# Optimization experiments

Hardware: AMD Instinct MI355X
Metric: run time of the kernel (lower is better)

## Reference

```python
import jax, jax.numpy as jnp
import numpy as np

# (multiplicity, dim=2l+1) per irreducible field, for both input and output
RS = [(8, 1), (8, 3), (8, 5)]
SIZE = 3          # conv kernel spatial size
B_EL = 2          # radial basis elements per (i,j) kernel block
EPS = 1e-5


def _se3_bn_conv(x, weight, bases):
    """Training-mode SE3BatchNorm stats fused into dynamic kernel build + conv3d.
    x: (B, C_in, D, H, W); weight: flat (sum mi*mj*b_el,);
    bases[i][j]: (b_el, di, dj, SIZE, SIZE, SIZE).
    """
    B = x.shape[0]
    means = []    # per scalar (d==1) field: (m,)
    scales = []   # per field: (m,) inverse-std factors
    ix = 0
    for m, d in RS:
        field = x[:, ix:ix + m * d].reshape(B, m, d, -1)
        ix += m * d
        if d == 1:
            mean = jax.lax.stop_gradient(field.mean(axis=-1).mean(axis=0).reshape(-1))
            field = field - mean.reshape(1, m, 1, 1)
            means.append(mean)
        # reduce='mean': sum over d, mean over spatial, mean over batch (detached)
        norm = jax.lax.stop_gradient(jnp.sum(field * field, axis=2).mean(axis=-1).mean(axis=0))
        scales.append((norm + EPS) ** -0.5)

    # Build normalized dynamic kernel blocks and compensating bias
    widx = 0
    row_blocks = []
    bias_parts = []
    for i, (mi, di) in enumerate(RS):
        col_blocks = []
        bia = jnp.zeros((mi * di,), x.dtype)
        imean = 0
        for j, (mj, dj) in enumerate(RS):
            basis = bases[i][j]                     # (b, di, dj, s, s, s)
            b = basis.shape[0]
            w = weight[widx:widx + mi * mj * b].reshape(mi, mj, b)
            widx += mi * mj * b
            w = w * scales[j][None, :, None]        # per-input-field BN rescale
            # block: (mi*di, mj*dj, s, s, s)
            block = jnp.einsum('uvb,bdexyz->udvexyz', w, basis)
            col_blocks.append(block.reshape(mi * di, mj * dj, SIZE, SIZE, SIZE))
            if di == 1 and dj == 1:
                mean = means[imean]
                imean += 1
                identity = basis.reshape(b, -1).sum(-1)         # (b,)
                corr = (w.reshape(-1, b) @ identity[:, None]).reshape(mi, mj)
                bia = bia - (corr @ mean[:, None]).reshape(-1)
        row_blocks.append(jnp.concatenate(col_blocks, axis=1))
        bias_parts.append(bia)
    kernel = jnp.concatenate(row_blocks, axis=0)    # (C_out, C_in, s, s, s)
    bias = jnp.concatenate(bias_parts)              # (C_out,)

    out = jax.lax.conv_general_dilated(
        x, kernel, window_strides=(1, 1, 1), padding='VALID',
        dimension_numbers=('NCDHW', 'OIDHW', 'NCDHW'))
    return out + bias[None, :, None, None, None]


def setup_inputs() -> dict:
    key = jax.random.key(0)
    k_x, k_w = jax.random.split(key)
    C = sum(m * d for m, d in RS)  # 72
    x = jax.random.normal(k_x, (8, C, 32, 32, 32), jnp.float32)
    total_w = sum(mi * mj * B_EL for mi, _ in RS for mj, _ in RS)  # 1152
    weight = jax.random.normal(k_w, (total_w,), jnp.float32) * 0.1
    inp = {'x': x, 'weight': weight}
    for i, (mi, di) in enumerate(RS):
        for j, (mj, dj) in enumerate(RS):
            kb = jax.random.fold_in(key, 100 + 10 * i + j)
            inp['basis_{}_{}'.format(i, j)] = jax.random.normal(
                kb, (B_EL, di, dj, SIZE, SIZE, SIZE), jnp.float32) / (SIZE ** 1.5)
    return inp


def reference(x, weight, basis_0_0, basis_0_1, basis_0_2,
              basis_1_0, basis_1_1, basis_1_2,
              basis_2_0, basis_2_1, basis_2_2):
    bases = [[basis_0_0, basis_0_1, basis_0_2],
             [basis_1_0, basis_1_1, basis_1_2],
             [basis_2_0, basis_2_1, basis_2_2]]
    return _se3_bn_conv(x, weight, bases)
```

## Files before the change

kernel.cpp:

```cpp
#include <hip/hip_runtime.h>
#include <hip/hip_fp16.h>
#include <math.h>

#define NCH 72
#define SP  32768
#define NBATCH 8
#define NTOT (NBATCH*SP)

#define WS_SUMX   0
#define WS_SUMSQ  72
#define WS_SCALE  144
#define WS_BIAS   216
#define WS_K      288

#define WS_XH_BYTES 323712
#define XH_ROW   2720
#define XH_PLANE 87040
#define XH_BATCH 2785280

typedef __attribute__((ext_vector_type(8))) _Float16 half8;
typedef __attribute__((ext_vector_type(4))) float float4v;
typedef __attribute__((ext_vector_type(4))) int int4v;

__device__ __forceinline__ void chmap(int c, int& f, int& m, int& d, int& dim) {
  if (c < 8)       { f = 0; m = c;          d = 0;          dim = 1; }
  else if (c < 32) { f = 1; m = (c - 8)/3;  d = (c - 8)%3;  dim = 3; }
  else             { f = 2; m = (c - 32)/5; d = (c - 32)%5; dim = 5; }
}

__global__ __launch_bounds__(256) void prepack_kernel(const float* __restrict__ x,
                                                      float* __restrict__ ws) {
  __shared__ __align__(16) short tile[256 * 88];
  __shared__ float segS[72][3], segQ[72][3];
  const int t    = threadIdx.x;
  const int z    = blockIdx.x >> 1;
  const int half = blockIdx.x & 1;
  const int b    = blockIdx.y;
  ushort* xh = (ushort*)((char*)ws + WS_XH_BYTES);
  const float* xb = x + (size_t)b * NCH * SP + z * 1024 + half * 512;

  const int ci_s = t % 72, seg = t / 72;
  float accS = 0.f, accQ = 0.f;

  *(int4v*)&tile[t * 88 + 72] = (int4v){0, 0, 0, 0};

  for (int c = 0; c < 2; ++c) {
    if (c) __syncthreads();
    #pragma unroll
    for (int cig = 0; cig < 18; ++cig) {
      float v0 = xb[(size_t)(cig*4 + 0) * SP + c * 256 + t];
      float v1 = xb[(size_t)(cig*4 + 1) * SP + c * 256 + t];
      float v2 = xb[(size_t)(cig*4 + 2) * SP + c * 256 + t];
      float v3 = xb[(size_t)(cig*4 + 3) * SP + c * 256 + t];
      short s4[4] = { (short)__half_as_short(__float2half(v0)),
                      (short)__half_as_short(__float2half(v1)),
                      (short)__half_as_short(__float2half(v2)),
                      (short)__half_as_short(__float2half(v3)) };
      *(int2*)&tile[t * 88 + cig * 4] = *(const int2*)s4;
    }
    __syncthreads();
    {
      ushort* gb = xh + (size_t)b * XH_BATCH + (size_t)(z * 32 + (half * 2 + c) * 8) * XH_ROW;
      #pragma unroll
      for (int j = 0; j < 10; ++j) {
        const int s   = t + j * 256;
        const int pos = s / 10, part = s - pos * 10;
        const int4v v = *(const int4v*)&tile[pos * 88 + part * 8];
        const int row = pos >> 5, xx = pos & 31;
        *(int4v*)(gb + (size_t)row * XH_ROW + xx * 80 + part * 8) = v;
      }
    }
    if (seg < 3) {
      const int p0 = seg * 86;
      const int pn = (seg == 2) ? 84 : 86;
      for (int i = 0; i < pn; ++i) {
        const float v = __half2float(__short_as_half(tile[(p0 + i) * 88 + ci_s]));
        accS += v; accQ += v * v;
      }
    }
  }
  if (seg < 3) { segS[ci_s][seg] = accS; segQ[ci_s][seg] = accQ; }
  __syncthreads();
  if (t < 144) {
    const int which = t / 72, ci = t % 72;
    const float v = which ? (segQ[ci][0] + segQ[ci][1] + segQ[ci][2])
                          : (segS[ci][0] + segS[ci][1] + segS[ci][2]);
    atomicAdd(&ws[(which ? WS_SUMSQ : WS_SUMX) + ci], v);
  }
}

__global__ __launch_bounds__(256) void build_half_kernel(const float* __restrict__ weight,
    float* __restrict__ ws,
    const float* __restrict__ b00, const float* __restrict__ b01, const float* __restrict__ b02,
    const float* __restrict__ b10, const float* __restrict__ b11, const float* __restrict__ b12,
    const float* __restrict__ b20, const float* __restrict__ b21, const float* __restrict__ b22) {
  const int tid = blockIdx.x * 256 + threadIdx.x;
  const float invN = 1.0f / (float)NTOT;
  if (tid < 315 * 512) {
    const int blk = tid >> 9;
    const int e   = tid & 511;
    const int tap = blk / 35;
    const int r   = blk - tap * 35;
    const int kc  = r / 5, cj = r - (r / 5) * 5;
    const int l   = e >> 3, j = e & 7;
    const int co  = cj * 16 + (l & 15);
    const int kk  = kc * 32 + ((l >> 4) << 3) + j;
    short val = 0;
    if (co < NCH && kk < 216) {
      const int dx = kk / 72, ci = kk - dx * 72;
      int fi, u, dd, di; chmap(co, fi, u, dd, di);
      int fj, v, ee, dj; chmap(ci, fj, v, ee, dj);
      const float* bs[9] = {b00, b01, b02, b10, b11, b12, b20, b21, b22};
      const float* basis = bs[fi * 3 + fj];
      float norm;
      if (ci < 8) {
        float m = ws[WS_SUMX + ci] * invN;
        norm = ws[WS_SUMSQ + ci] * invN - m * m;
      } else if (ci < 32) {
        int m0 = 8 + ((ci - 8) / 3) * 3;
        norm = (ws[WS_SUMSQ+m0] + ws[WS_SUMSQ+m0+1] + ws[WS_SUMSQ+m0+2]) * invN;
      } else {
        int m0 = 32 + ((ci - 32) / 5) * 5;
        norm = (ws[WS_SUMSQ+m0] + ws[WS_SUMSQ+m0+1] + ws[WS_SUMSQ+m0+2]
              + ws[WS_SUMSQ+m0+3] + ws[WS_SUMSQ+m0+4]) * invN;
      }
      const float sc = 1.0f / sqrtf(norm + 1e-5f);
      const float* wp = weight + (fi * 3 + fj) * 128 + (u * 8 + v) * 2;
      const float w0 = wp[0] * sc, w1 = wp[1] * sc;
      const int t = tap * 3 + dx;
      const float f = w0 * basis[(dd * dj + ee) * 27 + t]
                    + w1 * basis[((di + dd) * dj + ee) * 27 + t];
      val = __half_as_short(__float2half(f));
    }
    ((short*)(ws + WS_K))[tid] = val;
  }
  if (blockIdx.x == 0) {
    __shared__ float s_mean[8], s_scale[8];
    const int c = threadIdx.x;
    if (c < 8) {
      float m = ws[WS_SUMX + c] * invN;
      float norm = ws[WS_SUMSQ + c] * invN - m * m;
      s_mean[c]  = m;
      s_scale[c] = 1.0f / sqrtf(norm + 1e-5f);
    }
    __syncthreads();
    if (c < NCH) {
      float bia = 0.f;
      if (c < 8) {
        float id0 = 0.f, id1 = 0.f;
        #pragma unroll
        for (int t = 0; t < 27; ++t) { id0 += b00[t]; id1 += b00[27 + t]; }
        #pragma unroll
        for (int v = 0; v < 8; ++v) {
          float s  = s_scale[v];
          float w0 = weight[(c*8 + v)*2 + 0] * s;
          float w1 = weight[(c*8 + v)*2 + 1] * s;
          bia -= (w0 * id0 + w1 * id1) * s_mean[v];
        }
      }
      ws[WS_BIAS + c] = bia;
    }
  }
}

__global__ __launch_bounds__(256, 2) void conv_direct(const float* __restrict__ ws,
                                                      float* __restrict__ out) {
  __shared__ __align__(16) char Bsm[35840];

  const int lane = threadIdx.x & 63;
  const int wv   = threadIdx.x >> 6;
  const int lx   = lane & 15;
  const int q    = lane >> 4;
  const int i  = blockIdx.x;
  const int b  = i & 7;
  const int q2 = i >> 3;
  const int yt = q2 & 7;
  const int zp = q2 >> 3;
  const int y  = yt * 4 + wv;
  const int yc = (y > 29) ? 29 : y;
  const int zb = zp * 2;

  const char* xhb = (const char*)ws + WS_XH_BYTES + (size_t)b * (XH_BATCH * 2);
  const char* Kb  = (const char*)(ws + WS_K);
  const float* __restrict__ bias = ws + WS_BIAS;

  const int lb16 = lane * 16;

  float4v acc[2][2][5];
  #pragma unroll
  for (int sz = 0; sz < 2; ++sz)
    #pragma unroll
    for (int s = 0; s < 2; ++s)
      #pragma unroll
      for (int cj = 0; cj < 5; ++cj)
        acc[sz][s][cj] = (float4v){0.f, 0.f, 0.f, 0.f};

#define STAGE(TAP) {                                                              \
    const char* src_ = Kb + (size_t)(TAP) * 35840;                                \
    _Pragma("unroll")                                                             \
    for (int k = 0; k < 9; ++k) {                                                 \
      const int idx = (int)threadIdx.x + (k << 8);                                \
      if (idx < 2240) {                                                           \
        __builtin_amdgcn_global_load_lds(                                         \
          (const __attribute__((address_space(1))) void*)(src_ + (size_t)idx*16), \
          (__attribute__((address_space(3))) void*)(Bsm + ((k<<8) + (wv<<6))*16), \
          16, 0, 0);                                                              \
      }                                                                           \
    }                                                                             \
  }

#define LOADA(KC, A) {                                                            \
    const int kk0_ = (KC) * 32 + (q << 3);                                        \
    const int dx_  = (kk0_ >= 144) ? 2 : ((kk0_ >= 72) ? 1 : 0);                  \
    const int ao_  = (lx * 80 + kk0_ + 8 * dx_) * 2;                              \
    A[0] = *(const half8*)(r0T + ao_);                                            \
    A[1] = *(const half8*)(r0T + ao_ + 2560);                                     \
    A[2] = *(const half8*)(r1T + ao_);                                            \
    A[3] = *(const half8*)(r1T + ao_ + 2560);                                     \
  }

#define MFQ(A, BF, CJ)                                                                         \
    acc[0][0][CJ] = __builtin_amdgcn_mfma_f32_16x16x32_f16(A[0], BF, acc[0][0][CJ], 0,0,0);    \
    acc[0][1][CJ] = __builtin_amdgcn_mfma_f32_16x16x32_f16(A[1], BF, acc[0][1][CJ], 0,0,0);    \
    acc[1][0][CJ] = __builtin_amdgcn_mfma_f32_16x16x32_f16(A[2], BF, acc[1][0][CJ], 0,0,0);    \
    acc[1][1][CJ] = __builtin_amdgcn_mfma_f32_16x16x32_f16(A[3], BF, acc[1][1][CJ], 0,0,0);

#define GROUP(KC, AC, PRE) {                                                      \
    half8 bf0 = *(const half8*)(Bsm + ((KC)*5 + 0)*1024 + lb16);                  \
    half8 bf1 = *(const half8*)(Bsm + ((KC)*5 + 1)*1024 + lb16);                  \
    half8 bf2 = *(const half8*)(Bsm + ((KC)*5 + 2)*1024 + lb16);                  \
    half8 bf3 = *(const half8*)(Bsm + ((KC)*5 + 3)*1024 + lb16);                  \
    half8 bf4 = *(const half8*)(Bsm + ((KC)*5 + 4)*1024 + lb16);                  \
    PRE;                                                                          \
    __builtin_amdgcn_s_setprio(1);                                                \
    MFQ(AC, bf0, 0) MFQ(AC, bf1, 1) MFQ(AC, bf2, 2) MFQ(AC, bf3, 3) MFQ(AC, bf4, 4) \
    __builtin_amdgcn_s_setprio(0);                                                \
  }

  half8 A0[4], A1[4], A2[4];

  #pragma unroll 1
  for (int tap = 0; tap < 9; ++tap) {
    const int dz_ = tap / 3, dy_ = tap - dz_ * 3;
    const char* r0T = xhb + (size_t)(((zb + dz_) * 32) + (yc + dy_)) * (XH_ROW * 2);
    const char* r1T = r0T + (XH_PLANE * 2);

    if (tap) __builtin_amdgcn_s_barrier();
    STAGE(tap);
    __builtin_amdgcn_sched_barrier(0);
    LOADA(0, A0); LOADA(1, A1);
    __builtin_amdgcn_sched_barrier(0);
    asm volatile("s_waitcnt vmcnt(8)" ::: "memory");
    __builtin_amdgcn_s_barrier();
    __builtin_amdgcn_sched_barrier(0);

    GROUP(0, A0, LOADA(2, A2));
    GROUP(1, A1, LOADA(3, A0));
    GROUP(2, A2, LOADA(4, A1));
    GROUP(3, A0, LOADA(5, A2));
    GROUP(4, A1, LOADA(6, A0));
    GROUP(5, A2, (void)0);
    GROUP(6, A0, (void)0);
  }

#undef STAGE
#undef LOADA
#undef MFQ
#undef GROUP

  if (y < 30) {
    #pragma unroll
    for (int cj = 0; cj < 5; ++cj) {
      const int co = cj * 16 + lx;
      if (co < NCH) {
        const float bv = bias[co];
        #pragma unroll
        for (int sz = 0; sz < 2; ++sz) {
          float* ob = out + ((size_t)(b * NCH + co) * 30 + (zb + sz)) * 900 + y * 30;
          #pragma unroll
          for (int s = 0; s < 2; ++s) {
            const int x0 = s * 16 + q * 4;
            const float4v v = acc[sz][s][cj];
            float2 p0; p0.x = v[0] + bv; p0.y = v[1] + bv;
            *(float2*)(ob + x0) = p0;
            if (x0 + 2 < 30) {
              float2 p1; p1.x = v[2] + bv; p1.y = v[3] + bv;
              *(float2*)(ob + x0 + 2) = p1;
            }
          }
        }
      }
    }
  }
}

extern "C" void kernel_launch(void* const* d_in, const int* in_sizes, int n_in,
                              void* d_out, int out_size, void* d_ws, size_t ws_size,
                              hipStream_t stream) {
  const float* x = (const float*)d_in[0];
  const float* w = (const float*)d_in[1];
  const float* bs[9];
  for (int i = 0; i < 9; ++i) bs[i] = (const float*)d_in[2 + i];
  float* ws  = (float*)d_ws;
  float* out = (float*)d_out;

  hipMemsetAsync(d_ws, 0, 144 * sizeof(float), stream);

  prepack_kernel<<<dim3(64, NBATCH), 256, 0, stream>>>(x, ws);
  build_half_kernel<<<(315 * 512 + 255) / 256, 256, 0, stream>>>(
      w, ws, bs[0], bs[1], bs[2], bs[3], bs[4], bs[5], bs[6], bs[7], bs[8]);
  conv_direct<<<dim3(960), 256, 0, stream>>>(ws, out);
}
```

Baseline: 255.9 us.

## Double-buffer weight taps in LDS and prefetch next tap's operands

The conv kernel now keeps two LDS buffers for weight taps, so the load of tap t+1 into LDS is issued while tap t is being computed. It also starts loading the next tap's first activation fragments, and register-prefetches the B fragments one group ahead. This removes the per-tap barrier stall in which the whole block waited for the weight stage before any MFMA work. The cost is twice the LDS (70 KB per block, dynamic), which may limit how many blocks fit on a CU, plus higher register pressure under launch_bounds(256,2).

```diff
diff --git a/kernel.cpp b/kernel.cpp
--- a/kernel.cpp
+++ b/kernel.cpp
@@ -165,7 +165,7 @@
 
 __global__ __launch_bounds__(256, 2) void conv_direct(const float* __restrict__ ws,
                                                       float* __restrict__ out) {
-  __shared__ __align__(16) char Bsm[35840];
+  extern __shared__ __align__(16) char Bsm[];
 
   const int lane = threadIdx.x & 63;
   const int wv   = threadIdx.x >> 6;
@@ -195,28 +195,37 @@
       for (int cj = 0; cj < 5; ++cj)
         acc[sz][s][cj] = (float4v){0.f, 0.f, 0.f, 0.f};
 
-#define STAGE(TAP) {                                                              \
+#define STAGE(TAP, BUF) {                                                         \
     const char* src_ = Kb + (size_t)(TAP) * 35840;                                \
+    char* dst_ = Bsm + (size_t)(BUF) * 35840;                                     \
     _Pragma("unroll")                                                             \
     for (int k = 0; k < 9; ++k) {                                                 \
       const int idx = (int)threadIdx.x + (k << 8);                                \
       if (idx < 2240) {                                                           \
         __builtin_amdgcn_global_load_lds(                                         \
           (const __attribute__((address_space(1))) void*)(src_ + (size_t)idx*16), \
-          (__attribute__((address_space(3))) void*)(Bsm + ((k<<8) + (wv<<6))*16), \
+          (__attribute__((address_space(3))) void*)(dst_ + ((k<<8) + (wv<<6))*16),\
           16, 0, 0);                                                              \
       }                                                                           \
     }                                                                             \
   }
 
-#define LOADA(KC, A) {                                                            \
+#define LOADA(R0, R1, KC, A) {                                                    \
     const int kk0_ = (KC) * 32 + (q << 3);                                        \
     const int dx_  = (kk0_ >= 144) ? 2 : ((kk0_ >= 72) ? 1 : 0);                  \
     const int ao_  = (lx * 80 + kk0_ + 8 * dx_) * 2;                              \
-    A[0] = *(const half8*)(r0T + ao_);                                            \
-    A[1] = *(const half8*)(r0T + ao_ + 2560);                                     \
-    A[2] = *(const half8*)(r1T + ao_);                                            \
-    A[3] = *(const half8*)(r1T + ao_ + 2560);                                     \
+    A[0] = *(const half8*)((R0) + ao_);                                           \
+    A[1] = *(const half8*)((R0) + ao_ + 2560);                                    \
+    A[2] = *(const half8*)((R1) + ao_);                                           \
+    A[3] = *(const half8*)((R1) + ao_ + 2560);                                    \
+  }
+
+#define BPRE(BC, KC, BQ) {                                                        \
+    BQ[0] = *(const half8*)((BC) + ((KC)*5 + 0)*1024 + lb16);                     \
+    BQ[1] = *(const half8*)((BC) + ((KC)*5 + 1)*1024 + lb16);                     \
+    BQ[2] = *(const half8*)((BC) + ((KC)*5 + 2)*1024 + lb16);                     \
+    BQ[3] = *(const half8*)((BC) + ((KC)*5 + 3)*1024 + lb16);                     \
+    BQ[4] = *(const half8*)((BC) + ((KC)*5 + 4)*1024 + lb16);                     \
   }
 
 #define MFQ(A, BF, CJ)                                                                         \
@@ -225,48 +234,62 @@
     acc[1][0][CJ] = __builtin_amdgcn_mfma_f32_16x16x32_f16(A[2], BF, acc[1][0][CJ], 0,0,0);    \
     acc[1][1][CJ] = __builtin_amdgcn_mfma_f32_16x16x32_f16(A[3], BF, acc[1][1][CJ], 0,0,0);
 
-#define GROUP(KC, AC, PRE) {                                                      \
-    half8 bf0 = *(const half8*)(Bsm + ((KC)*5 + 0)*1024 + lb16);                  \
-    half8 bf1 = *(const half8*)(Bsm + ((KC)*5 + 1)*1024 + lb16);                  \
-    half8 bf2 = *(const half8*)(Bsm + ((KC)*5 + 2)*1024 + lb16);                  \
-    half8 bf3 = *(const half8*)(Bsm + ((KC)*5 + 3)*1024 + lb16);                  \
-    half8 bf4 = *(const half8*)(Bsm + ((KC)*5 + 4)*1024 + lb16);                  \
-    PRE;                                                                          \
+#define MFMAG(A, BQ) {                                                            \
     __builtin_amdgcn_s_setprio(1);                                                \
-    MFQ(AC, bf0, 0) MFQ(AC, bf1, 1) MFQ(AC, bf2, 2) MFQ(AC, bf3, 3) MFQ(AC, bf4, 4) \
+    MFQ(A, BQ[0], 0) MFQ(A, BQ[1], 1) MFQ(A, BQ[2], 2) MFQ(A, BQ[3], 3) MFQ(A, BQ[4], 4) \
     __builtin_amdgcn_s_setprio(0);                                                \
   }
 
-  half8 A0[4], A1[4], A2[4];
+#define TAPBODY(TT, X, Y, Z) {                                                    \
+    const int T_  = (TT);                                                         \
+    const int dz_ = T_ / 3, dy_ = T_ - 3 * dz_;                                   \
+    const char* r0T = xhb + (size_t)(((zb + dz_) * 32) + (yc + dy_)) * (XH_ROW*2);\
+    const char* r1T = r0T + (XH_PLANE * 2);                                       \
+    const char* Bc  = Bsm + (size_t)(T_ & 1) * 35840;                             \
+    BPRE(Bc, 0, Bq0);                                                             \
+    if (T_ < 8) STAGE(T_ + 1, ((T_ + 1) & 1));                                    \
+    const int Tn_  = (T_ < 8) ? T_ + 1 : T_;                                      \
+    const int dzn_ = Tn_ / 3, dyn_ = Tn_ - 3 * dzn_;                              \
+    const char* rn0 = xhb + (size_t)(((zb + dzn_) * 32) + (yc + dyn_)) * (XH_ROW*2);\
+    const char* rn1 = rn0 + (XH_PLANE * 2);                                       \
+    BPRE(Bc, 1, Bq1); LOADA(r0T, r1T, 2, Z);  MFMAG(X, Bq0);                      \
+    BPRE(Bc, 2, Bq0); LOADA(r0T, r1T, 3, X);  MFMAG(Y, Bq1);                      \
+    BPRE(Bc, 3, Bq1); LOADA(r0T, r1T, 4, Y);  MFMAG(Z, Bq0);                      \
+    BPRE(Bc, 4, Bq0); LOADA(r0T, r1T, 5, Z);  MFMAG(X, Bq1);                      \
+    BPRE(Bc, 5, Bq1); LOADA(r0T, r1T, 6, X);  MFMAG(Y, Bq0);                      \
+    BPRE(Bc, 6, Bq0); if (T_ < 8) LOADA(rn0, rn1, 0, Y);  MFMAG(Z, Bq1);          \
+    if (T_ < 8) LOADA(rn0, rn1, 1, Z);  MFMAG(X, Bq0);                            \
+    if (T_ < 8) {                                                                 \
+      asm volatile("s_waitcnt vmcnt(8)" ::: "memory");                            \
+      __builtin_amdgcn_s_barrier();                                               \
+    }                                                                             \
+  }
+
+  half8 A0[4], A1[4], A2[4], Bq0[5], Bq1[5];
+
+  STAGE(0, 0);
+  {
+    const char* r0P = xhb + (size_t)((zb * 32) + yc) * (XH_ROW * 2);
+    const char* r1P = r0P + (XH_PLANE * 2);
+    LOADA(r0P, r1P, 0, A0);
+    LOADA(r0P, r1P, 1, A1);
+  }
+  asm volatile("s_waitcnt vmcnt(8)" ::: "memory");
+  __builtin_amdgcn_s_barrier();
 
   #pragma unroll 1
-  for (int tap = 0; tap < 9; ++tap) {
-    const int dz_ = tap / 3, dy_ = tap - dz_ * 3;
-    const char* r0T = xhb + (size_t)(((zb + dz_) * 32) + (yc + dy_)) * (XH_ROW * 2);
-    const char* r1T = r0T + (XH_PLANE * 2);
-
-    if (tap) __builtin_amdgcn_s_barrier();
-    STAGE(tap);
-    __builtin_amdgcn_sched_barrier(0);
-    LOADA(0, A0); LOADA(1, A1);
-    __builtin_amdgcn_sched_barrier(0);
-    asm volatile("s_waitcnt vmcnt(8)" ::: "memory");
-    __builtin_amdgcn_s_barrier();
-    __builtin_amdgcn_sched_barrier(0);
-
-    GROUP(0, A0, LOADA(2, A2));
-    GROUP(1, A1, LOADA(3, A0));
-    GROUP(2, A2, LOADA(4, A1));
-    GROUP(3, A0, LOADA(5, A2));
-    GROUP(4, A1, LOADA(6, A0));
-    GROUP(5, A2, (void)0);
-    GROUP(6, A0, (void)0);
+  for (int s3 = 0; s3 < 9; s3 += 3) {
+    TAPBODY(s3 + 0, A0, A1, A2)
+    TAPBODY(s3 + 1, A1, A2, A0)
+    TAPBODY(s3 + 2, A2, A0, A1)
   }
 
 #undef STAGE
 #undef LOADA
+#undef BPRE
 #undef MFQ
-#undef GROUP
+#undef MFMAG
+#undef TAPBODY
 
   if (y < 30) {
     #pragma unroll
@@ -309,5 +332,5 @@
   prepack_kernel<<<dim3(64, NBATCH), 256, 0, stream>>>(x, ws);
   build_half_kernel<<<(315 * 512 + 255) / 256, 256, 0, stream>>>(
       w, ws, bs[0], bs[1], bs[2], bs[3], bs[4], bs[5], bs[6], bs[7], bs[8]);
-  conv_direct<<<dim3(960), 256, 0, stream>>>(ws, out);
-}
+  conv_direct<<<dim3(960), 256, 71680, stream>>>(ws, out);
+}
```

After: 255.9 us. About the same (-0.0%).
